# Kernel tuning notes

Measured on AMD Instinct MI355X. Metric: run time of the kernel, lower is better.

Reference implementation:

```python
import jax, jax.numpy as jnp
import numpy as np

C = 256
CQ = C // 8  # query/key channels


def setup_inputs() -> dict:
    key = jax.random.key(0)
    ks = jax.random.split(key, 8)
    B, H, W = 4, 64, 64
    x = jax.random.normal(ks[0], (B, C, H, W), dtype=jnp.float32)
    mask = jax.random.uniform(ks[1], (B, 1, H, W), dtype=jnp.float32)
    # 1x1 conv weights stored as [out_ch, in_ch] (kernel_size=1)
    s = 1.0 / np.sqrt(C)
    Wq = jax.random.uniform(ks[2], (CQ, C), dtype=jnp.float32, minval=-s, maxval=s)
    bq = jax.random.uniform(ks[3], (CQ,), dtype=jnp.float32, minval=-s, maxval=s)
    Wk = jax.random.uniform(ks[4], (CQ, C), dtype=jnp.float32, minval=-s, maxval=s)
    bk = jax.random.uniform(ks[5], (CQ,), dtype=jnp.float32, minval=-s, maxval=s)
    Wv = jax.random.uniform(ks[6], (C, C), dtype=jnp.float32, minval=-s, maxval=s)
    bv = jax.random.uniform(ks[7], (C,), dtype=jnp.float32, minval=-s, maxval=s)
    gamma = jnp.ones((1,), dtype=jnp.float32)
    return {"x": x, "mask": mask, "Wq": Wq, "bq": bq, "Wk": Wk, "bk": bk,
            "Wv": Wv, "bv": bv, "gamma": gamma}


def reference(x, mask, Wq, bq, Wk, bk, Wv, bv, gamma):
    B, Cc, H, W = x.shape
    N = H * W
    xf = x.reshape(B, Cc, N)                  # [B, C, N]
    m = mask.reshape(B, 1, N)                 # [B, 1, N]
    # 1x1 convs == per-pixel linear maps over channels
    q = jnp.einsum('oc,bcn->bon', Wq, xf) + bq[None, :, None]  # [B, CQ, N]
    k = jnp.einsum('oc,bcn->bon', Wk, xf) + bk[None, :, None]  # [B, CQ, N]
    v = jnp.einsum('oc,bcn->bon', Wv, xf) + bv[None, :, None]  # [B, C,  N]
    q = q * m
    k = k * m
    energy = jnp.einsum('bci,bcj->bij', q, k)  # [B, N, N] (queries x keys)
    attn = jax.nn.softmax(energy, axis=-1)
    out = jnp.einsum('bcj,bij->bci', v, attn)  # [B, C, N]
    out = out.reshape(B, Cc, H, W)
    return gamma * out + x
```

## Files before the change

kernel.cpp:

```cpp
#include <hip/hip_runtime.h>
#include <math.h>

#define CC 256
#define NPIX 4096
#define BATCH 4
#define LOG2E 1.4426950408889634f

typedef __attribute__((ext_vector_type(8)))  short short8;
typedef __attribute__((ext_vector_type(8)))  int   int32x8;
typedef __attribute__((ext_vector_type(16))) float f32x16;

union FragU { short8 v; short s[8]; unsigned u[4]; uint2 d[2]; };
union V8  { uint4 q[2]; int32x8 iv; };
union B8  { unsigned u[8]; int32x8 iv; };

__device__ inline unsigned pkbf(float a, float b) {
    unsigned x = __float_as_uint(a), y = __float_as_uint(b);
    x = (x + 0x7FFFu + ((x >> 16) & 1u)) >> 16;
    y = (y + 0x7FFFu + ((y >> 16) & 1u)) & 0xFFFF0000u;
    return x | y;
}
__device__ inline unsigned short bf1(float a) {
    unsigned x = __float_as_uint(a);
    return (unsigned short)((x + 0x7FFFu + ((x >> 16) & 1u)) >> 16);
}
__device__ inline float ex2(float x) { return __builtin_amdgcn_exp2f(x); }
__device__ inline unsigned pk4fp8(float a, float b, float c, float d) {
    int r = __builtin_amdgcn_cvt_pk_fp8_f32(a, b, 0, false);
    r = __builtin_amdgcn_cvt_pk_fp8_f32(c, d, r, true);
    return (unsigned)r;
}
__device__ inline f32x16 zero16() {
    f32x16 v;
    #pragma unroll
    for (int i = 0; i < 16; ++i) v[i] = 0.0f;
    return v;
}
__device__ inline f32x16 mfma32(short8 a, short8 b, f32x16 c) {
    return __builtin_amdgcn_mfma_f32_32x32x16_bf16(a, b, c, 0, 0, 0);
}
__device__ inline f32x16 mfma64s(int32x8 a, int32x8 b, f32x16 c) {
    return __builtin_amdgcn_mfma_scale_f32_32x32x64_f8f6f4(
        a, b, c, 0 , 0 , 0, 0x7F, 0, 0x7F);
}

__global__ __launch_bounds__(256, 2) void prep_kernel(
    const float* __restrict__ x,
    const float* __restrict__ Wq, const float* __restrict__ Wk,
    const float* __restrict__ Wv,
    unsigned short* __restrict__ xT, unsigned short* __restrict__ Wfrag)
{
    const int t = threadIdx.x;
    const int bid = blockIdx.x;
    if (bid < 256) {
        __shared__ unsigned short xs[256 * 68];
        const int b = bid >> 6, u = bid & 63;
        const int p0 = u * 64;
        const float* xb = x + (size_t)b * CC * NPIX + p0;
        #pragma unroll
        for (int k = 0; k < 16; ++k) {
            int c = (t >> 4) + 16 * k;
            int p4 = (t & 15) * 4;
            float4 v = *(const float4*)(xb + (size_t)c * NPIX + p4);
            *(uint2*)&xs[c * 68 + p4] = make_uint2(pkbf(v.x, v.y), pkbf(v.z, v.w));
        }
        __syncthreads();
        const int w = t >> 6, l = t & 63;
        const int c8 = l & 31;
        #pragma unroll
        for (int i = 0; i < 8; ++i) {
            int p = i * 8 + w * 2 + (l >> 5);
            unsigned short tmp[8];
            #pragma unroll
            for (int j = 0; j < 8; ++j) tmp[j] = xs[(c8 * 8 + j) * 68 + p];
            uint4 o;
            o.x = tmp[0] | ((unsigned)tmp[1] << 16);
            o.y = tmp[2] | ((unsigned)tmp[3] << 16);
            o.z = tmp[4] | ((unsigned)tmp[5] << 16);
            o.w = tmp[6] | ((unsigned)tmp[7] << 16);
            *(uint4*)(xT + (size_t)(b * NPIX + p0 + p) * 256 + c8 * 8) = o;
        }
    } else {
        const int wb = bid - 256;
        const int l = t & 63, rr = t >> 6;
        #pragma unroll
        for (int e = 0; e < 4; ++e) {
            int gs = wb * 4 + e;
            int g = gs >> 4, s = gs & 15;
            const float* src; float scale = 1.0f; int oc0 = 0;
            if (g == 0)      { src = Wq; scale = LOG2E; }
            else if (g == 1) { src = Wk; }
            else             { src = Wv; oc0 = (g - 2) * 32; }
            int row = oc0 + (l & 31);
            int kb2 = 16 * s + 8 * (l >> 5) + rr * 2;
            float v0 = src[(size_t)row * CC + kb2] * scale;
            float v1 = src[(size_t)row * CC + kb2 + 1] * scale;
            *(unsigned*)(Wfrag + (size_t)(gs * 64 + l) * 8 + rr * 2) = pkbf(v0, v1);
        }
    }
}

__global__ __launch_bounds__(320, 3) void proj_mfma(
    const unsigned short* __restrict__ xT, const unsigned short* __restrict__ Wfrag,
    const float* __restrict__ mask,
    const float* __restrict__ bq, const float* __restrict__ bk,
    const float* __restrict__ bv,
    unsigned short* __restrict__ qT, unsigned short* __restrict__ kT,
    unsigned char* __restrict__ vI)
{
    __shared__ unsigned short xls[64 * 260];
    const int t = threadIdx.x;
    const int w = t >> 6, l = t & 63, L = l & 31, h = l >> 5;
    const int bid = blockIdx.x;
    const int b    = (bid >> 1) & 3;
    const int u    = ((bid >> 3) << 1) | (bid & 1);
    const int p0   = (u >> 1) * 64;
    const int half = u & 1;
    const int ocg  = half * 5 + w;

    const unsigned short* xg = xT + (size_t)(b * NPIX + p0) * 256;
    #pragma unroll
    for (int r = 0; r < 7; ++r) {
        int idx = r * 2560 + t * 8;
        if (idx < 16384) {
            uint4 d = *(const uint4*)(xg + idx);
            int p = idx >> 8, c = idx & 255;
            *(uint2*)&xls[p * 260 + c]     = make_uint2(d.x, d.y);
            *(uint2*)&xls[p * 260 + c + 4] = make_uint2(d.z, d.w);
        }
    }

    FragU wf[16];
    const unsigned short* wp = Wfrag + (size_t)(ocg * 16 * 64 + l) * 8;
    #pragma unroll
    for (int s = 0; s < 16; ++s) wf[s].v = *(const short8*)(wp + s * 512);

    float bcol;
    if (ocg == 0)      bcol = bq[L] * LOG2E;
    else if (ocg == 1) bcol = bk[L];
    else               bcol = bv[(ocg - 2) * 32 + L];
    const float* mb = mask + (size_t)b * NPIX;
    __syncthreads();

    #pragma unroll
    for (int mt = 0; mt < 2; ++mt) {
        const int pp = 32 * mt;
        f32x16 acc = zero16();
        #pragma unroll
        for (int s = 0; s < 16; ++s) {
            FragU af;
            const unsigned short* ap = &xls[(pp + L) * 260 + 16 * s + 8 * h];
            af.d[0] = *(const uint2*)(ap);
            af.d[1] = *(const uint2*)(ap + 4);
            acc = mfma32(af.v, wf[s].v, acc);
        }
        if (ocg < 2) {
            unsigned short* dst = (ocg ? kT : qT) + (size_t)b * NPIX * 32;
            #pragma unroll
            for (int r = 0; r < 16; ++r) {
                int prow = (r & 3) + 8 * (r >> 2) + 4 * h;
                float mv = mb[p0 + pp + prow];
                dst[(size_t)(p0 + pp + prow) * 32 + L] = bf1((acc[r] + bcol) * mv);
            }
        } else {
            const int cg = ocg - 2;
            const int jb32 = p0 + pp;
            unsigned char* dst = vI + (size_t)b * (1 << 20)
                + (size_t)(jb32 >> 6) * 16384 + cg * 2048
                + (((jb32 >> 5) & 1) * 32 + L) * 32 + 4 * h;
            #pragma unroll
            for (int m = 0; m < 4; ++m) {
                unsigned pk = pk4fp8(acc[4*m]   + bcol, acc[4*m+1] + bcol,
                                     acc[4*m+2] + bcol, acc[4*m+3] + bcol);
                *(unsigned*)(dst + 8 * m) = pk;
            }
        }
    }
}

__global__ __launch_bounds__(256, 2) void attn_mfma(
    const unsigned short* __restrict__ qT, const unsigned short* __restrict__ kT,
    const unsigned char* __restrict__ vI, const float* __restrict__ x,
    const float* __restrict__ gamma, float* __restrict__ out)
{
    __shared__ float mls[2][4][32];
    __shared__ float obuf[4][2048];

    const int t = threadIdx.x;
    const int w = t >> 6, l = t & 63, L = l & 31, h = l >> 5;
    const int bid = blockIdx.x;
    const int b  = (bid >> 1) & 3;
    const int it = (bid >> 3) * 2 + (bid & 1);
    const int i0 = it * 32;

    const unsigned short* qrow = qT + ((size_t)b * NPIX + i0 + L) * 32 + 8 * h;
    short8 qf0 = *(const short8*)(qrow);
    short8 qf1 = *(const short8*)(qrow + 16);

    const int jbase = w * 1024;
    const unsigned char* kp = (const unsigned char*)kT
        + (size_t)b * NPIX * 64 + (size_t)jbase * 64 + (size_t)L * 64 + 16 * h;
    short8 ka0 = *(const short8*)(kp);
    short8 ka1 = *(const short8*)(kp + 32);
    short8 kb0 = *(const short8*)(kp + 2048);
    short8 kb1 = *(const short8*)(kp + 2080);
    kp += 4096;
    const unsigned char* vp = vI + (size_t)b * (1 << 20)
        + (size_t)(jbase >> 6) * 16384 + (size_t)l * 32;

    f32x16 acc[8];
    #pragma unroll
    for (int cg = 0; cg < 8; ++cg) acc[cg] = zero16();
    float m_run = -INFINITY, l_run = 0.0f;

    for (int itr = 0; itr < 16; ++itr) {
        f32x16 s0 = zero16(), s1 = zero16();
        s0 = mfma32(ka0, qf0, s0);
        s0 = mfma32(ka1, qf1, s0);
        s1 = mfma32(kb0, qf0, s1);
        s1 = mfma32(kb1, qf1, s1);

        ka0 = *(const short8*)(kp);
        ka1 = *(const short8*)(kp + 32);
        kb0 = *(const short8*)(kp + 2048);
        kb1 = *(const short8*)(kp + 2080);
        kp += 4096;

        V8 vv[4];
        #pragma unroll
        for (int cg = 0; cg < 4; ++cg) {
            vv[cg].q[0] = *(const uint4*)(vp + cg * 2048);
            vv[cg].q[1] = *(const uint4*)(vp + cg * 2048 + 16);
        }

        float t0 = s0[0], t1 = s0[1], t2 = s0[2], t3 = s0[3];
        #pragma unroll
        for (int r = 4; r < 16; r += 4) {
            t0 = fmaxf(t0, s0[r]);     t1 = fmaxf(t1, s0[r + 1]);
            t2 = fmaxf(t2, s0[r + 2]); t3 = fmaxf(t3, s0[r + 3]);
        }
        #pragma unroll
        for (int r = 0; r < 16; r += 4) {
            t0 = fmaxf(t0, s1[r]);     t1 = fmaxf(t1, s1[r + 1]);
            t2 = fmaxf(t2, s1[r + 2]); t3 = fmaxf(t3, s1[r + 3]);
        }
        float tmax = fmaxf(fmaxf(t0, t1), fmaxf(t2, t3));
        tmax = fmaxf(tmax, __shfl_xor(tmax, 32));
        if (__ballot(tmax > m_run + 3.0f)) {
            float m_new = fmaxf(m_run, tmax);
            float alpha = ex2(m_run - m_new);
            l_run *= alpha;
            #pragma unroll
            for (int cg = 0; cg < 8; ++cg)
                #pragma unroll
                for (int r = 0; r < 16; ++r) acc[cg][r] *= alpha;
            m_run = m_new;
        }

        float z0 = 0, z1 = 0, z2 = 0, z3 = 0;
        #pragma unroll
        for (int r = 0; r < 16; r += 4) {
            s0[r]   = ex2(s0[r]   - m_run); z0 += s0[r];
            s0[r+1] = ex2(s0[r+1] - m_run); z1 += s0[r+1];
            s0[r+2] = ex2(s0[r+2] - m_run); z2 += s0[r+2];
            s0[r+3] = ex2(s0[r+3] - m_run); z3 += s0[r+3];
        }
        #pragma unroll
        for (int r = 0; r < 16; r += 4) {
            s1[r]   = ex2(s1[r]   - m_run); z0 += s1[r];
            s1[r+1] = ex2(s1[r+1] - m_run); z1 += s1[r+1];
            s1[r+2] = ex2(s1[r+2] - m_run); z2 += s1[r+2];
            s1[r+3] = ex2(s1[r+3] - m_run); z3 += s1[r+3];
        }
        float ssum = (z0 + z1) + (z2 + z3);
        ssum += __shfl_xor(ssum, 32);
        l_run += ssum;

        unsigned u0[4], u1[4], p0[4], p1[4];
        #pragma unroll
        for (int m = 0; m < 4; ++m) {
            u0[m] = pk4fp8(s0[4*m], s0[4*m+1], s0[4*m+2], s0[4*m+3]);
            u1[m] = pk4fp8(s1[4*m], s1[4*m+1], s1[4*m+2], s1[4*m+3]);
        }
        #pragma unroll
        for (int q = 0; q < 4; ++q) {
            p0[q] = (unsigned)__shfl_xor((int)u0[q], 32);
            p1[q] = (unsigned)__shfl_xor((int)u1[q], 32);
        }
        B8 bf;
        #pragma unroll
        for (int m = 0; m < 4; ++m) {
            unsigned oh = h ? u1[m] : u0[m];
            unsigned ph = h ? p1[m] : p0[m];
            bf.u[2*m]     = h ? ph : oh;
            bf.u[2*m + 1] = h ? oh : ph;
        }

        #pragma unroll
        for (int cg = 0; cg < 4; ++cg) acc[cg] = mfma64s(vv[cg].iv, bf.iv, acc[cg]);
        #pragma unroll
        for (int cg = 0; cg < 4; ++cg) {
            vv[cg].q[0] = *(const uint4*)(vp + (cg + 4) * 2048);
            vv[cg].q[1] = *(const uint4*)(vp + (cg + 4) * 2048 + 16);
        }
        #pragma unroll
        for (int cg = 0; cg < 4; ++cg) acc[cg + 4] = mfma64s(vv[cg].iv, bf.iv, acc[cg + 4]);
        vp += 16384;
    }

    if (h == 0) { mls[0][w][L] = m_run; mls[1][w][L] = l_run; }
    __syncthreads();
    float m0 = mls[0][0][L], m1 = mls[0][1][L], m2 = mls[0][2][L], m3 = mls[0][3][L];
    float ms = fmaxf(fmaxf(m0, m1), fmaxf(m2, m3));
    float f0 = ex2(m0 - ms), f1 = ex2(m1 - ms);
    float f2 = ex2(m2 - ms), f3 = ex2(m3 - ms);
    float lstar = f0 * mls[1][0][L] + f1 * mls[1][1][L]
                + f2 * mls[1][2][L] + f3 * mls[1][3][L];
    float fw = (w == 0) ? f0 : (w == 1) ? f1 : (w == 2) ? f2 : f3;
    const float scale = gamma[0] / lstar;

    #pragma unroll
    for (int cg = 0; cg < 8; ++cg)
        #pragma unroll
        for (int r = 0; r < 16; ++r) acc[cg][r] *= fw;

    const int ti = t & 31, trow = t >> 5;
    for (int ck = 0; ck < 4; ++ck) {
        #pragma unroll
        for (int half = 0; half < 2; ++half) {
            #pragma unroll
            for (int r = 0; r < 16; ++r) {
                int prow = (r & 3) + 8 * (r >> 2) + 4 * h;
                obuf[w][half * 1024 + prow * 32 + L] = acc[2 * ck + half][r];
            }
        }
        __syncthreads();
        #pragma unroll
        for (int rr = 0; rr < 8; ++rr) {
            int cr = trow + 8 * rr;
            int idx = cr * 32 + ti;
            float sum = obuf[0][idx] + obuf[1][idx] + obuf[2][idx] + obuf[3][idx];
            size_t gi = ((size_t)b * CC + ck * 64 + cr) * NPIX + i0 + ti;
            out[gi] = scale * sum + x[gi];
        }
        __syncthreads();
    }
}

extern "C" void kernel_launch(void* const* d_in, const int* in_sizes, int n_in,
                              void* d_out, int out_size, void* d_ws, size_t ws_size,
                              hipStream_t stream) {
    const float* x     = (const float*)d_in[0];
    const float* mask  = (const float*)d_in[1];
    const float* Wq    = (const float*)d_in[2];
    const float* bq    = (const float*)d_in[3];
    const float* Wk    = (const float*)d_in[4];
    const float* bk    = (const float*)d_in[5];
    const float* Wv    = (const float*)d_in[6];
    const float* bv    = (const float*)d_in[7];
    const float* gamma = (const float*)d_in[8];
    float* out = (float*)d_out;

    unsigned short* ws = (unsigned short*)d_ws;
    unsigned short* qT = ws;
    unsigned short* kT = qT + (size_t)BATCH * NPIX * 32;
    unsigned char*  vI = (unsigned char*)(kT + (size_t)BATCH * NPIX * 32);
    unsigned short* xT = (unsigned short*)(vI + (size_t)BATCH * CC * NPIX);
    unsigned short* Wfrag = xT + (size_t)BATCH * NPIX * 256;

    prep_kernel<<<296, 256, 0, stream>>>(x, Wq, Wk, Wv, xT, Wfrag);
    proj_mfma<<<512, 320, 0, stream>>>(xT, Wfrag, mask, bq, bk, bv, qT, kT, vI);
    attn_mfma<<<512, 256, 0, stream>>>(qT, kT, vI, x, gamma, out);
}
```

Measured before the change: 135.0 us.

## Swizzle prep LDS transpose, add MFMA priority hints, skip first rescale, fold merge weights

```diff
diff --git a/kernel.cpp b/kernel.cpp
--- a/kernel.cpp
+++ b/kernel.cpp
@@ -61,18 +61,21 @@
         for (int k = 0; k < 16; ++k) {
             int c = (t >> 4) + 16 * k;
             int p4 = (t & 15) * 4;
+            int p4s = p4 ^ (((c >> 3) & 15) << 2);
             float4 v = *(const float4*)(xb + (size_t)c * NPIX + p4);
-            *(uint2*)&xs[c * 68 + p4] = make_uint2(pkbf(v.x, v.y), pkbf(v.z, v.w));
+            *(uint2*)&xs[c * 68 + p4s] = make_uint2(pkbf(v.x, v.y), pkbf(v.z, v.w));
         }
         __syncthreads();
         const int w = t >> 6, l = t & 63;
         const int c8 = l & 31;
+        const int psw = ((c8 & 15) << 2);
         #pragma unroll
         for (int i = 0; i < 8; ++i) {
             int p = i * 8 + w * 2 + (l >> 5);
+            int ps = p ^ psw;
             unsigned short tmp[8];
             #pragma unroll
-            for (int j = 0; j < 8; ++j) tmp[j] = xs[(c8 * 8 + j) * 68 + p];
+            for (int j = 0; j < 8; ++j) tmp[j] = xs[(c8 * 8 + j) * 68 + ps];
             uint4 o;
             o.x = tmp[0] | ((unsigned)tmp[1] << 16);
             o.y = tmp[2] | ((unsigned)tmp[3] << 16);
@@ -212,13 +215,16 @@
     #pragma unroll
     for (int cg = 0; cg < 8; ++cg) acc[cg] = zero16();
     float m_run = -INFINITY, l_run = 0.0f;
+    bool warm = false;
 
     for (int itr = 0; itr < 16; ++itr) {
         f32x16 s0 = zero16(), s1 = zero16();
+        __builtin_amdgcn_s_setprio(1);
         s0 = mfma32(ka0, qf0, s0);
         s0 = mfma32(ka1, qf1, s0);
         s1 = mfma32(kb0, qf0, s1);
         s1 = mfma32(kb1, qf1, s1);
+        __builtin_amdgcn_s_setprio(0);
 
         ka0 = *(const short8*)(kp);
         ka1 = *(const short8*)(kp + 32);
@@ -233,28 +239,37 @@
             vv[cg].q[1] = *(const uint4*)(vp + cg * 2048 + 16);
         }
 
-        float t0 = s0[0], t1 = s0[1], t2 = s0[2], t3 = s0[3];
-        #pragma unroll
-        for (int r = 4; r < 16; r += 4) {
-            t0 = fmaxf(t0, s0[r]);     t1 = fmaxf(t1, s0[r + 1]);
-            t2 = fmaxf(t2, s0[r + 2]); t3 = fmaxf(t3, s0[r + 3]);
-        }
-        #pragma unroll
-        for (int r = 0; r < 16; r += 4) {
-            t0 = fmaxf(t0, s1[r]);     t1 = fmaxf(t1, s1[r + 1]);
-            t2 = fmaxf(t2, s1[r + 2]); t3 = fmaxf(t3, s1[r + 3]);
-        }
-        float tmax = fmaxf(fmaxf(t0, t1), fmaxf(t2, t3));
+        float t0 = fmaxf(fmaxf(s0[0],  s0[4]),  s0[8]);
+        float t1 = fmaxf(fmaxf(s0[1],  s0[5]),  s0[9]);
+        float t2 = fmaxf(fmaxf(s0[2],  s0[6]),  s0[10]);
+        float t3 = fmaxf(fmaxf(s0[3],  s0[7]),  s0[11]);
+        t0 = fmaxf(fmaxf(t0, s0[12]), s1[0]);
+        t1 = fmaxf(fmaxf(t1, s0[13]), s1[1]);
+        t2 = fmaxf(fmaxf(t2, s0[14]), s1[2]);
+        t3 = fmaxf(fmaxf(t3, s0[15]), s1[3]);
+        t0 = fmaxf(fmaxf(t0, s1[4]),  s1[8]);
+        t1 = fmaxf(fmaxf(t1, s1[5]),  s1[9]);
+        t2 = fmaxf(fmaxf(t2, s1[6]),  s1[10]);
+        t3 = fmaxf(fmaxf(t3, s1[7]),  s1[11]);
+        t0 = fmaxf(t0, s1[12]);
+        t1 = fmaxf(t1, s1[13]);
+        t2 = fmaxf(t2, s1[14]);
+        t3 = fmaxf(t3, s1[15]);
+        float tmax = fmaxf(fmaxf(fmaxf(t0, t1), t2), t3);
         tmax = fmaxf(tmax, __shfl_xor(tmax, 32));
+
         if (__ballot(tmax > m_run + 3.0f)) {
             float m_new = fmaxf(m_run, tmax);
-            float alpha = ex2(m_run - m_new);
-            l_run *= alpha;
-            #pragma unroll
-            for (int cg = 0; cg < 8; ++cg)
+            if (warm) {
+                float alpha = ex2(m_run - m_new);
+                l_run *= alpha;
                 #pragma unroll
-                for (int r = 0; r < 16; ++r) acc[cg][r] *= alpha;
+                for (int cg = 0; cg < 8; ++cg)
+                    #pragma unroll
+                    for (int r = 0; r < 16; ++r) acc[cg][r] *= alpha;
+            }
             m_run = m_new;
+            warm = true;
         }
 
         float z0 = 0, z1 = 0, z2 = 0, z3 = 0;
@@ -296,6 +311,7 @@
             bf.u[2*m + 1] = h ? oh : ph;
         }
 
+        __builtin_amdgcn_s_setprio(1);
         #pragma unroll
         for (int cg = 0; cg < 4; ++cg) acc[cg] = mfma64s(vv[cg].iv, bf.iv, acc[cg]);
         #pragma unroll
@@ -305,24 +321,21 @@
         }
         #pragma unroll
         for (int cg = 0; cg < 4; ++cg) acc[cg + 4] = mfma64s(vv[cg].iv, bf.iv, acc[cg + 4]);
+        __builtin_amdgcn_s_setprio(0);
         vp += 16384;
     }
 
     if (h == 0) { mls[0][w][L] = m_run; mls[1][w][L] = l_run; }
     __syncthreads();
     float m0 = mls[0][0][L], m1 = mls[0][1][L], m2 = mls[0][2][L], m3 = mls[0][3][L];
-    float ms = fmaxf(fmaxf(m0, m1), fmaxf(m2, m3));
+    float ms = fmaxf(fmaxf(fmaxf(m0, m1), m2), m3);
     float f0 = ex2(m0 - ms), f1 = ex2(m1 - ms);
     float f2 = ex2(m2 - ms), f3 = ex2(m3 - ms);
     float lstar = f0 * mls[1][0][L] + f1 * mls[1][1][L]
                 + f2 * mls[1][2][L] + f3 * mls[1][3][L];
-    float fw = (w == 0) ? f0 : (w == 1) ? f1 : (w == 2) ? f2 : f3;
     const float scale = gamma[0] / lstar;
-
-    #pragma unroll
-    for (int cg = 0; cg < 8; ++cg)
-        #pragma unroll
-        for (int r = 0; r < 16; ++r) acc[cg][r] *= fw;
+    const float g0 = scale * f0, g1 = scale * f1;
+    const float g2 = scale * f2, g3 = scale * f3;
 
     const int ti = t & 31, trow = t >> 5;
     for (int ck = 0; ck < 4; ++ck) {
@@ -339,9 +352,10 @@
         for (int rr = 0; rr < 8; ++rr) {
             int cr = trow + 8 * rr;
             int idx = cr * 32 + ti;
-            float sum = obuf[0][idx] + obuf[1][idx] + obuf[2][idx] + obuf[3][idx];
+            float sum = g0 * obuf[0][idx] + g1 * obuf[1][idx]
+                      + g2 * obuf[2][idx] + g3 * obuf[3][idx];
             size_t gi = ((size_t)b * CC + ck * 64 + cr) * NPIX + i0 + ti;
-            out[gi] = scale * sum + x[gi];
+            out[gi] = sum + x[gi];
         }
         __syncthreads();
     }
```

New measurement: 128.5 us. -4.8%, faster.
